# Optimization experiments

Measured on AMD Instinct MI355X. Metric: run time of the kernel, lower is better.

The kernel has to match this reference:

```python
import jax, jax.numpy as jnp
import numpy as np

EMBED_DIM = 1024
NUM_HEADS = 16
HEAD_DIM = EMBED_DIM // NUM_HEADS
SCALE = HEAD_DIM ** -0.5
B, S = 2, 2048


def setup_inputs() -> dict:
    key = jax.random.key(0)
    ks = jax.random.split(key, 11)
    lim = 1.0 / np.sqrt(EMBED_DIM)
    def lin(kw, kb):
        W = jax.random.uniform(kw, (EMBED_DIM, EMBED_DIM), jnp.float32, -lim, lim)
        b = jax.random.uniform(kb, (EMBED_DIM,), jnp.float32, -lim, lim)
        return W, b
    Wq, bq = lin(ks[0], ks[1])
    Wk, bk = lin(ks[2], ks[3])
    Wv, bv = lin(ks[4], ks[5])
    Wo, bo = lin(ks[6], ks[7])
    query = jax.random.normal(ks[8], (B, S, EMBED_DIM), jnp.float32)
    key_t = jax.random.normal(ks[9], (B, S, EMBED_DIM), jnp.float32)
    value = jax.random.normal(ks[10], (B, S, EMBED_DIM), jnp.float32)
    return {"query": query, "key": key_t, "value": value,
            "Wq": Wq, "bq": bq, "Wk": Wk, "bk": bk,
            "Wv": Wv, "bv": bv, "Wo": Wo, "bo": bo}


def reference(query, key, value, Wq, bq, Wk, bk, Wv, bv, Wo, bo):
    # 'flash' path with attn_mask=None == full softmax attention (chunking is
    # only an execution schedule; per-chunk softmax is over the full key axis).
    b, s, _ = query.shape
    def heads(x, W, bias):
        y = x @ W.T + bias                      # [b, s, E]
        return y.reshape(b, s, NUM_HEADS, HEAD_DIM).transpose(0, 2, 1, 3)  # [b, h, s, d]
    q = heads(query, Wq, bq)
    k = heads(key, Wk, bk)
    v = heads(value, Wv, bv)
    scores = jnp.einsum('bhqd,bhkd->bhqk', q, k) * SCALE
    attn = jax.nn.softmax(scores, axis=-1)
    out = jnp.einsum('bhqk,bhkd->bhqd', attn, v)
    out = out.transpose(0, 2, 1, 3).reshape(b, s, EMBED_DIM)
    return out @ Wo.T + bo
```

## Files before the change

kernel.cpp:

```cpp
#include <hip/hip_runtime.h>

typedef unsigned short u16;
typedef unsigned int u32;
typedef __attribute__((ext_vector_type(8))) __bf16 bf16x8;
typedef __attribute__((ext_vector_type(4))) float f32x4;
typedef __attribute__((ext_vector_type(4))) unsigned short u16x4;
typedef __attribute__((ext_vector_type(8))) unsigned short u16x8;
typedef __attribute__((ext_vector_type(2))) unsigned int u32x2;
typedef __attribute__((ext_vector_type(4))) unsigned int u32x4;

#define DEV static __device__ __forceinline__

DEV void async_copy16(const void* g, void* l) {
  __builtin_amdgcn_global_load_lds((const __attribute__((address_space(1))) void*)g,
                                   (__attribute__((address_space(3))) void*)l, 16, 0, 0);
}
DEV float b2f(u16 s) { union { unsigned u; float f; } v; v.u = ((unsigned)s) << 16; return v.f; }
DEV u16 f2b(float f) {
  union { float f; unsigned u; } v; v.f = f;
  unsigned r = v.u + 0x7FFFu + ((v.u >> 16) & 1u);
  return (u16)(r >> 16);
}
DEV u32 pack2bf(float a, float b) {
  u32 ua = __float_as_uint(a) + 0x8000u;
  u32 ub = __float_as_uint(b) + 0x8000u;
  return __builtin_amdgcn_perm(ub, ua, 0x07060302u);
}

#define MFMA(a, b, c) __builtin_amdgcn_mfma_f32_16x16x32_bf16((a), (b), (c), 0, 0, 0)

__global__ void detect_dtype(const unsigned* __restrict__ q, int* __restrict__ flag) {
  const int lane = threadIdx.x;
  const unsigned w = q[lane];
  const unsigned e = (w >> 7) & 0xFFu;
  const bool inr = (e >= 100u && e <= 132u);
  const unsigned long long m = __ballot(inr);
  if (lane == 0) flag[0] = (__popcll(m) >= 48) ? 1 : 0;
}

__global__ void convert_inputs(
    const void* s0, const void* s1, const void* s2,
    const void* s3, const void* s4, const void* s5, const void* s6,
    const void* s7, const void* s8, const void* s9, const void* s10,
    u16* __restrict__ d0, u16* __restrict__ d1, u16* __restrict__ d2,
    u16* __restrict__ d3, u16* __restrict__ d4, u16* __restrict__ d5, u16* __restrict__ d6,
    float* __restrict__ e7, float* __restrict__ e8, float* __restrict__ e9, float* __restrict__ e10,
    const int* __restrict__ flag)
{
  const int bi = blockIdx.y;
  const void* src = nullptr; u16* db = nullptr; float* df = nullptr; int n = 0;
  switch (bi) {
    case 0:  src = s0;  db = d0; n = 4194304; break;
    case 1:  src = s1;  db = d1; n = 4194304; break;
    case 2:  src = s2;  db = d2; n = 4194304; break;
    case 3:  src = s3;  db = d3; n = 1048576; break;
    case 4:  src = s4;  db = d4; n = 1048576; break;
    case 5:  src = s5;  db = d5; n = 1048576; break;
    case 6:  src = s6;  db = d6; n = 1048576; break;
    case 7:  src = s7;  df = e7; n = 1024; break;
    case 8:  src = s8;  df = e8; n = 1024; break;
    case 9:  src = s9;  df = e9; n = 1024; break;
    default: src = s10; df = e10; n = 1024; break;
  }
  const int isbf = flag[0];
  const int stride = gridDim.x * 256 * 8;
  for (int i = (blockIdx.x * 256 + threadIdx.x) * 8; i < n; i += stride) {
    if (db) {
      u16x8 v;
      if (isbf) {
        v = *(const u16x8*)((const u16*)src + i);
      } else {
        const float* sf = (const float*)src;
#pragma unroll
        for (int j = 0; j < 8; ++j) v[j] = f2b(sf[i + j]);
      }
      *(u16x8*)(db + i) = v;
    } else {
#pragma unroll
      for (int j = 0; j < 8; ++j) {
        float x = isbf ? b2f(((const u16*)src)[i + j]) : ((const float*)src)[i + j];
        df[i + j] = x;
      }
    }
  }
}

__global__ void gemm_qkv(const u16* __restrict__ X0, const u16* __restrict__ X1, const u16* __restrict__ X2,
                         const u16* __restrict__ W0, const u16* __restrict__ W1, const u16* __restrict__ W2,
                         const float* __restrict__ B0, const float* __restrict__ B1, const float* __restrict__ B2,
                         u16* __restrict__ Y0, u16* __restrict__ Y1, u16* __restrict__ Y2,
                         float* __restrict__ Yf, const int* __restrict__ flag, int mode0)
{
  __shared__ __align__(16) u16 smem[17408];

  const int z = blockIdx.z;
  const u16* X  = (z == 0) ? X0 : ((z == 1) ? X1 : X2);
  const u16* W  = (z == 0) ? W0 : ((z == 1) ? W1 : W2);
  const float* Bi = (z == 0) ? B0 : ((z == 1) ? B1 : B2);
  u16* Y        = (z == 0) ? Y0 : ((z == 1) ? Y1 : Y2);
  const int mode = mode0 ? mode0 : z;
  const int outbf = flag[0];

  const int t = threadIdx.x, wave = t >> 6, lane = t & 63;
  const int lane15 = lane & 15, quad = lane >> 4;

  const int L = blockIdx.y * 8 + blockIdx.x;
  const int wrk = (L & 7) * 32 + (L >> 3);
  const int m0 = (wrk >> 3) * 128, n0 = (wrk & 7) * 128;

  const u16* gA = X + (size_t)(m0 + wave * 16 + (lane >> 2)) * 1024 + (lane & 3) * 8;
  const u16* gB = W + (size_t)(n0 + wave * 16 + (lane >> 2)) * 1024 + (lane & 3) * 8;

  f32x4 acc[4][4];
#pragma unroll
  for (int i = 0; i < 4; ++i)
#pragma unroll
    for (int j = 0; j < 4; ++j) acc[i][j] = (f32x4){0.f, 0.f, 0.f, 0.f};

  const int wr = wave >> 1, wc = wave & 1;

  u16* lA0 = smem + wave * 512;
  u16* lB0 = smem + 4096 + wave * 512;
  u16* lA1 = smem + 8192 + wave * 512;
  u16* lB1 = smem + 12288 + wave * 512;

  auto stage = [&](u16* lA, u16* lB) {
    async_copy16(gA, lA);
    async_copy16(gA + 64 * 1024, lA + 64 * 32);
    async_copy16(gB, lB);
    async_copy16(gB + 64 * 1024, lB + 64 * 32);
    gA += 32; gB += 32;
  };
  auto compute = [&](const u16* As_, const u16* Bs_) {
    bf16x8 af[4], bfv[4];
#pragma unroll
    for (int mt = 0; mt < 4; ++mt)
      af[mt] = *(const bf16x8*)&As_[(wr * 64 + mt * 16 + lane15) * 32 + quad * 8];
#pragma unroll
    for (int nt = 0; nt < 4; ++nt)
      bfv[nt] = *(const bf16x8*)&Bs_[(wc * 64 + nt * 16 + lane15) * 32 + quad * 8];
    __builtin_amdgcn_s_setprio(1);
#pragma unroll
    for (int mt = 0; mt < 4; ++mt)
#pragma unroll
      for (int nt = 0; nt < 4; ++nt)
        acc[mt][nt] = MFMA(af[mt], bfv[nt], acc[mt][nt]);
    __builtin_amdgcn_s_setprio(0);
  };

  stage(lA0, lB0);
  __syncthreads();

  for (int k0 = 0; k0 < 1024; k0 += 64) {
    if (k0 + 32 < 1024) stage(lA1, lB1);
    compute(smem, smem + 4096);
    __syncthreads();
    if (k0 + 64 < 1024) stage(lA0, lB0);
    compute(smem + 8192, smem + 12288);
    __syncthreads();
  }

  const float qscale = 0.125f * 1.44269504088896340736f;

  if (mode == 2) {
    u16* T2 = smem;
#pragma unroll
    for (int mt = 0; mt < 4; ++mt) {
      const int sl_base = wr * 64 + mt * 16 + quad * 4;
#pragma unroll
      for (int nt = 0; nt < 4; ++nt) {
        const int nn = wc * 64 + nt * 16 + lane15;
        const float bias_v = Bi[n0 + nn];
#pragma unroll
        for (int r = 0; r < 4; ++r) {
          const int sl = sl_base + r;
          T2[nn * 136 + sl] = f2b(acc[mt][nt][r] + bias_v);
        }
      }
    }
    __syncthreads();
    const size_t grow0 = (size_t)(m0 >> 11) * 1024 + n0;
    const int col0 = m0 & 2047;
#pragma unroll
    for (int i = 0; i < 8; ++i) {
      const int id = i * 256 + t;
      const int row = id >> 4, ch = id & 15;
      *(u16x8*)&Y[(grow0 + row) * 2048 + col0 + ch * 8] = *(const u16x8*)&T2[row * 136 + ch * 8];
    }
    return;
  }

#pragma unroll
  for (int mt = 0; mt < 4; ++mt) {
    const int m_base = m0 + wr * 64 + mt * 16 + quad * 4;
#pragma unroll
    for (int nt = 0; nt < 4; ++nt) {
      const int n = n0 + wc * 64 + nt * 16 + lane15;
      const float bias_v = Bi[n];
#pragma unroll
      for (int r = 0; r < 4; ++r) {
        const int m = m_base + r;
        float v = acc[mt][nt][r] + bias_v;
        if (mode == 0) v *= qscale;
        if (mode == 3) {
          if (outbf) Y[(size_t)m * 1024 + n] = f2b(v);
          else       Yf[(size_t)m * 1024 + n] = v;
        } else {
          size_t addr = (((size_t)(m >> 11) * 16 + (n >> 6)) * 2048 + (size_t)(m & 2047)) * 64 + (n & 63);
          Y[addr] = f2b(v);
        }
      }
    }
  }
}

__global__ __launch_bounds__(256, 4) void flash_attn(const u16* __restrict__ Qs, const u16* __restrict__ Ks,
                                                     const u16* __restrict__ Vt, u16* __restrict__ AO)
{
  __shared__ __align__(16) u16 smem[16384];
  u16* Kt = smem;
  u16* Vs = smem + 8192;

  const int t = threadIdx.x, wave = t >> 6, lane = t & 63;
  const int lane15 = lane & 15, quad = lane >> 4;
  const int l7 = lane15 & 7;

  const int Lb = blockIdx.y * 16 + blockIdx.x;
  const int wrk = (Lb & 7) * 64 + (Lb >> 3);
  const int bh = wrk >> 4;
  const int q0 = (wrk & 15) * 128;

  const u16* Qb = Qs + ((size_t)bh * 2048 + q0) * 64;
  const u16* Kb = Ks + (size_t)bh * 2048 * 64;
  const u16* Vb = Vt + (size_t)bh * 64 * 2048;

  const int krow = lane >> 3;
  const int kchunk = (lane & 7) ^ (krow & 7);
  const int vrow = lane >> 4;
  const int vchunk = (lane & 15) ^ (((wave & 1) << 2) + vrow);

#pragma unroll
  for (int r = 0; r < 4; ++r)
    async_copy16(Qb + (size_t)(r * 32 + wave * 8 + krow) * 64 + kchunk * 8,
                 &Kt[(r * 32 + wave * 8) * 64]);
  __syncthreads();
  bf16x8 aq[2][2];
#pragma unroll
  for (int mt = 0; mt < 2; ++mt)
#pragma unroll
    for (int ks = 0; ks < 2; ++ks)
      aq[mt][ks] = *(const bf16x8*)&Kt[(wave * 32 + mt * 16 + lane15) * 64 + ((ks * 4 + quad) ^ l7) * 8];
  __syncthreads();

  f32x4 acc_o[2][4], acc_l[2];
#pragma unroll
  for (int mt = 0; mt < 2; ++mt) {
    acc_l[mt] = (f32x4){0.f, 0.f, 0.f, 0.f};
#pragma unroll
    for (int i = 0; i < 4; ++i) acc_o[mt][i] = (f32x4){0.f, 0.f, 0.f, 0.f};
  }

  u16x8 ou;
#pragma unroll
  for (int j = 0; j < 8; ++j) ou[j] = 0x3F80;
  const bf16x8 ones = __builtin_bit_cast(bf16x8, ou);

  for (int kt = 0; kt < 16; ++kt) {
#pragma unroll
    for (int r = 0; r < 4; ++r)
      async_copy16(Kb + (size_t)(kt * 128 + r * 32 + wave * 8 + krow) * 64 + kchunk * 8,
                   &Kt[(r * 32 + wave * 8) * 64]);
#pragma unroll
    for (int r = 0; r < 4; ++r)
      async_copy16(Vb + (size_t)(r * 16 + wave * 4 + vrow) * 2048 + kt * 128 + vchunk * 8,
                   &Vs[(r * 16 + wave * 4) * 128]);
    __syncthreads();

#pragma unroll
    for (int ks2 = 0; ks2 < 4; ++ks2) {
      bf16x8 bk[2][2];
#pragma unroll
      for (int no = 0; no < 2; ++no)
#pragma unroll
        for (int ks = 0; ks < 2; ++ks)
          bk[no][ks] = *(const bf16x8*)&Kt[((ks2 * 2 + no) * 16 + lane15) * 64 + ((ks * 4 + quad) ^ l7) * 8];
      f32x4 s2[2][2];
#pragma unroll
      for (int mt = 0; mt < 2; ++mt)
#pragma unroll
        for (int no = 0; no < 2; ++no) s2[mt][no] = (f32x4){0.f, 0.f, 0.f, 0.f};
      __builtin_amdgcn_s_setprio(1);
#pragma unroll
      for (int mt = 0; mt < 2; ++mt)
#pragma unroll
        for (int no = 0; no < 2; ++no)
#pragma unroll
          for (int ks = 0; ks < 2; ++ks)
            s2[mt][no] = MFMA(bk[no][ks], aq[mt][ks], s2[mt][no]);
      __builtin_amdgcn_s_setprio(0);

      bf16x8 pa[2];
#pragma unroll
      for (int mt = 0; mt < 2; ++mt) {
        float e0[4], e1[4];
#pragma unroll
        for (int rg = 0; rg < 4; ++rg) {
          e0[rg] = __builtin_amdgcn_exp2f(s2[mt][0][rg]);
          e1[rg] = __builtin_amdgcn_exp2f(s2[mt][1][rg]);
        }
        const u32 x0 = pack2bf(e0[0], e0[1]), x1 = pack2bf(e0[2], e0[3]);
        const u32 y0 = pack2bf(e1[0], e1[1]), y1 = pack2bf(e1[2], e1[3]);
        const u32x2 rA = __builtin_amdgcn_permlane32_swap(x0, y0, false, false);
        const u32x2 rB = __builtin_amdgcn_permlane32_swap(x1, y1, false, false);
        const u32x2 f0 = __builtin_amdgcn_permlane16_swap(rA[0], rA[1], false, false);
        const u32x2 f1 = __builtin_amdgcn_permlane16_swap(rB[0], rB[1], false, false);
        const u32x4 paw = (u32x4){f0[0], f1[0], f0[1], f1[1]};
        pa[mt] = __builtin_bit_cast(bf16x8, paw);
      }

      bf16x8 bv[4];
#pragma unroll
      for (int dt = 0; dt < 4; ++dt)
        bv[dt] = *(const bf16x8*)&Vs[(dt * 16 + lane15) * 128 + ((ks2 * 4 + quad) ^ l7) * 8];
      __builtin_amdgcn_s_setprio(1);
#pragma unroll
      for (int mt = 0; mt < 2; ++mt) {
#pragma unroll
        for (int dt = 0; dt < 4; ++dt)
          acc_o[mt][dt] = MFMA(pa[mt], bv[dt], acc_o[mt][dt]);
        acc_l[mt] = MFMA(pa[mt], ones, acc_l[mt]);
      }
      __builtin_amdgcn_s_setprio(0);
    }
    __syncthreads();
  }

  float rinv[2][4];
#pragma unroll
  for (int mt = 0; mt < 2; ++mt)
#pragma unroll
    for (int rg = 0; rg < 4; ++rg) rinv[mt][rg] = 1.0f / acc_l[mt][rg];

  u16* T = smem;
#pragma unroll
  for (int mt = 0; mt < 2; ++mt)
#pragma unroll
    for (int dt = 0; dt < 4; ++dt)
#pragma unroll
      for (int rg = 0; rg < 4; ++rg)
        T[(wave * 32 + mt * 16 + quad * 4 + rg) * 72 + dt * 16 + lane15] =
            f2b(acc_o[mt][dt][rg] * rinv[mt][rg]);
  __syncthreads();

  const int b = bh >> 4, h = bh & 15;
#pragma unroll
  for (int i = 0; i < 4; ++i) {
    const int id = i * 256 + t;
    const int row = id >> 3, ch = id & 7;
    *(u16x8*)&AO[((size_t)b * 2048 + q0 + row) * 1024 + h * 64 + ch * 8] =
        *(const u16x8*)&T[row * 72 + ch * 8];
  }
}

extern "C" void kernel_launch(void* const* d_in, const int* in_sizes, int n_in,
                              void* d_out, int out_size, void* d_ws, size_t ws_size,
                              hipStream_t stream)
{
  const void* query = d_in[0];
  const void* key_  = d_in[1];
  const void* value = d_in[2];
  const void* Wq = d_in[3]; const void* bq = d_in[4];
  const void* Wk = d_in[5]; const void* bk = d_in[6];
  const void* Wv = d_in[7]; const void* bv = d_in[8];
  const void* Wo = d_in[9]; const void* bo = d_in[10];

  u16* ws = (u16*)d_ws;
  u16* Qs  = ws;
  u16* Ks  = Qs + 4194304;
  u16* Vt  = Ks + 4194304;
  u16* AO  = Vt + 4194304;
  u16* Xq  = AO + 4194304;
  u16* Xk  = Xq + 4194304;
  u16* Xv  = Xk + 4194304;
  u16* Wqc = Xv + 4194304;
  u16* Wkc = Wqc + 1048576;
  u16* Wvc = Wkc + 1048576;
  u16* Woc = Wvc + 1048576;
  float* Bc = (float*)(Woc + 1048576);
  int* flag = (int*)(Bc + 4096);

  detect_dtype<<<1, 64, 0, stream>>>((const unsigned*)query, flag);
  convert_inputs<<<dim3(128, 11), 256, 0, stream>>>(
      query, key_, value, Wq, Wk, Wv, Wo, bq, bk, bv, bo,
      Xq, Xk, Xv, Wqc, Wkc, Wvc, Woc,
      Bc, Bc + 1024, Bc + 2048, Bc + 3072, flag);

  gemm_qkv<<<dim3(8, 32, 3), 256, 0, stream>>>(Xq, Xk, Xv, Wqc, Wkc, Wvc,
                                               Bc, Bc + 1024, Bc + 2048,
                                               Qs, Ks, Vt, nullptr, flag, 0);
  flash_attn<<<dim3(16, 32), 256, 0, stream>>>(Qs, Ks, Vt, AO);
  gemm_qkv<<<dim3(8, 32, 1), 256, 0, stream>>>(AO, AO, AO, Woc, Woc, Woc,
                                               Bc + 3072, Bc + 3072, Bc + 3072,
                                               (u16*)d_out, (u16*)d_out, (u16*)d_out,
                                               (float*)d_out, flag, 3);
}
```

Before: 221.8 us.

## Split attention key tiles across wave pairs with doubled query rows per wave

Each wave now owns 64 query rows (instead of 32) and half of each 128-key tile. A pair of waves shares the same query rows and their partial O and row sums are reduced through shared memory at the end. This halves the K/V fragment LDS reads per unit of MFMA work, raising reuse of the loaded K and V fragments. In exchange it needs roughly double the accumulator registers (launch bounds lowered to 2 blocks per CU) and adds an end-of-kernel reduction with extra barriers.

```diff
diff --git a/kernel.cpp b/kernel.cpp
--- a/kernel.cpp
+++ b/kernel.cpp
@@ -214,7 +214,7 @@
   }
 }
 
-__global__ __launch_bounds__(256, 4) void flash_attn(const u16* __restrict__ Qs, const u16* __restrict__ Ks,
+__global__ __launch_bounds__(256, 2) void flash_attn(const u16* __restrict__ Qs, const u16* __restrict__ Ks,
                                                      const u16* __restrict__ Vt, u16* __restrict__ AO)
 {
   __shared__ __align__(16) u16 smem[16384];
@@ -224,6 +224,8 @@
   const int t = threadIdx.x, wave = t >> 6, lane = t & 63;
   const int lane15 = lane & 15, quad = lane >> 4;
   const int l7 = lane15 & 7;
+  const int h = wave >> 1;
+  const int c = wave & 1;
 
   const int Lb = blockIdx.y * 16 + blockIdx.x;
   const int wrk = (Lb & 7) * 64 + (Lb >> 3);
@@ -244,17 +246,18 @@
     async_copy16(Qb + (size_t)(r * 32 + wave * 8 + krow) * 64 + kchunk * 8,
                  &Kt[(r * 32 + wave * 8) * 64]);
   __syncthreads();
-  bf16x8 aq[2][2];
-#pragma unroll
-  for (int mt = 0; mt < 2; ++mt)
+  bf16x8 aq[4][2];
+#pragma unroll
+  for (int mt = 0; mt < 4; ++mt)
 #pragma unroll
     for (int ks = 0; ks < 2; ++ks)
-      aq[mt][ks] = *(const bf16x8*)&Kt[(wave * 32 + mt * 16 + lane15) * 64 + ((ks * 4 + quad) ^ l7) * 8];
-  __syncthreads();
-
-  f32x4 acc_o[2][4], acc_l[2];
-#pragma unroll
-  for (int mt = 0; mt < 2; ++mt) {
+      aq[mt][ks] = *(const bf16x8*)&Kt[(h * 64 + mt * 16 + lane15) * 64 + ((ks * 4 + quad) ^ l7) * 8];
+  __syncthreads();
+
+  f32x4 acc_o[4][4];
+  f32x4 acc_l[4];
+#pragma unroll
+  for (int mt = 0; mt < 4; ++mt) {
     acc_l[mt] = (f32x4){0.f, 0.f, 0.f, 0.f};
 #pragma unroll
     for (int i = 0; i < 4; ++i) acc_o[mt][i] = (f32x4){0.f, 0.f, 0.f, 0.f};
@@ -277,36 +280,34 @@
     __syncthreads();
 
 #pragma unroll
-    for (int ks2 = 0; ks2 < 4; ++ks2) {
+    for (int g = 0; g < 2; ++g) {
+      const int ks2 = c * 2 + g;
       bf16x8 bk[2][2];
 #pragma unroll
       for (int no = 0; no < 2; ++no)
 #pragma unroll
         for (int ks = 0; ks < 2; ++ks)
-          bk[no][ks] = *(const bf16x8*)&Kt[((ks2 * 2 + no) * 16 + lane15) * 64 + ((ks * 4 + quad) ^ l7) * 8];
-      f32x4 s2[2][2];
-#pragma unroll
-      for (int mt = 0; mt < 2; ++mt)
-#pragma unroll
-        for (int no = 0; no < 2; ++no) s2[mt][no] = (f32x4){0.f, 0.f, 0.f, 0.f};
-      __builtin_amdgcn_s_setprio(1);
-#pragma unroll
-      for (int mt = 0; mt < 2; ++mt)
+          bk[no][ks] = *(const bf16x8*)&Kt[(c * 64 + g * 32 + no * 16 + lane15) * 64 + ((ks * 4 + quad) ^ l7) * 8];
+
+      bf16x8 pa[4];
+#pragma unroll
+      for (int mt = 0; mt < 4; ++mt) {
+        f32x4 s2[2];
+        s2[0] = (f32x4){0.f, 0.f, 0.f, 0.f};
+        s2[1] = (f32x4){0.f, 0.f, 0.f, 0.f};
+        __builtin_amdgcn_s_setprio(1);
 #pragma unroll
         for (int no = 0; no < 2; ++no)
 #pragma unroll
           for (int ks = 0; ks < 2; ++ks)
-            s2[mt][no] = MFMA(bk[no][ks], aq[mt][ks], s2[mt][no]);
-      __builtin_amdgcn_s_setprio(0);
-
-      bf16x8 pa[2];
-#pragma unroll
-      for (int mt = 0; mt < 2; ++mt) {
+            s2[no] = MFMA(bk[no][ks], aq[mt][ks], s2[no]);
+        __builtin_amdgcn_s_setprio(0);
+
         float e0[4], e1[4];
 #pragma unroll
         for (int rg = 0; rg < 4; ++rg) {
-          e0[rg] = __builtin_amdgcn_exp2f(s2[mt][0][rg]);
-          e1[rg] = __builtin_amdgcn_exp2f(s2[mt][1][rg]);
+          e0[rg] = __builtin_amdgcn_exp2f(s2[0][rg]);
+          e1[rg] = __builtin_amdgcn_exp2f(s2[1][rg]);
         }
         const u32 x0 = pack2bf(e0[0], e0[1]), x1 = pack2bf(e0[2], e0[3]);
         const u32 y0 = pack2bf(e1[0], e1[1]), y1 = pack2bf(e1[2], e1[3]);
@@ -324,7 +325,7 @@
         bv[dt] = *(const bf16x8*)&Vs[(dt * 16 + lane15) * 128 + ((ks2 * 4 + quad) ^ l7) * 8];
       __builtin_amdgcn_s_setprio(1);
 #pragma unroll
-      for (int mt = 0; mt < 2; ++mt) {
+      for (int mt = 0; mt < 4; ++mt) {
 #pragma unroll
         for (int dt = 0; dt < 4; ++dt)
           acc_o[mt][dt] = MFMA(pa[mt], bv[dt], acc_o[mt][dt]);
@@ -335,29 +336,65 @@
     __syncthreads();
   }
 
-  float rinv[2][4];
-#pragma unroll
-  for (int mt = 0; mt < 2; ++mt)
-#pragma unroll
-    for (int rg = 0; rg < 4; ++rg) rinv[mt][rg] = 1.0f / acc_l[mt][rg];
+  float* Of = (float*)smem;
+  if (c == 1) {
+#pragma unroll
+    for (int mt = 0; mt < 4; ++mt)
+#pragma unroll
+      for (int dt = 0; dt < 4; ++dt)
+#pragma unroll
+        for (int rg = 0; rg < 4; ++rg)
+          Of[h * 4096 + (mt * 16 + quad * 4 + rg) * 64 + dt * 16 + lane15] = acc_o[mt][dt][rg];
+  }
+  __syncthreads();
+  if (c == 0) {
+#pragma unroll
+    for (int mt = 0; mt < 4; ++mt)
+#pragma unroll
+      for (int dt = 0; dt < 4; ++dt)
+#pragma unroll
+        for (int rg = 0; rg < 4; ++rg)
+          acc_o[mt][dt][rg] += Of[h * 4096 + (mt * 16 + quad * 4 + rg) * 64 + dt * 16 + lane15];
+  }
+  __syncthreads();
+  float* Lf = (float*)smem;
+  if (c == 1 && lane15 == 0) {
+#pragma unroll
+    for (int mt = 0; mt < 4; ++mt)
+#pragma unroll
+      for (int rg = 0; rg < 4; ++rg)
+        Lf[h * 64 + mt * 16 + quad * 4 + rg] = acc_l[mt][rg];
+  }
+  __syncthreads();
+  float rinv[4][4];
+  if (c == 0) {
+#pragma unroll
+    for (int mt = 0; mt < 4; ++mt)
+#pragma unroll
+      for (int rg = 0; rg < 4; ++rg)
+        rinv[mt][rg] = 1.0f / (acc_l[mt][rg] + Lf[h * 64 + mt * 16 + quad * 4 + rg]);
+  }
+  __syncthreads();
 
   u16* T = smem;
-#pragma unroll
-  for (int mt = 0; mt < 2; ++mt)
-#pragma unroll
-    for (int dt = 0; dt < 4; ++dt)
-#pragma unroll
-      for (int rg = 0; rg < 4; ++rg)
-        T[(wave * 32 + mt * 16 + quad * 4 + rg) * 72 + dt * 16 + lane15] =
-            f2b(acc_o[mt][dt][rg] * rinv[mt][rg]);
-  __syncthreads();
-
-  const int b = bh >> 4, h = bh & 15;
+  if (c == 0) {
+#pragma unroll
+    for (int mt = 0; mt < 4; ++mt)
+#pragma unroll
+      for (int dt = 0; dt < 4; ++dt)
+#pragma unroll
+        for (int rg = 0; rg < 4; ++rg)
+          T[(h * 64 + mt * 16 + quad * 4 + rg) * 72 + dt * 16 + lane15] =
+              f2b(acc_o[mt][dt][rg] * rinv[mt][rg]);
+  }
+  __syncthreads();
+
+  const int b = bh >> 4, hh = bh & 15;
 #pragma unroll
   for (int i = 0; i < 4; ++i) {
     const int id = i * 256 + t;
     const int row = id >> 3, ch = id & 7;
-    *(u16x8*)&AO[((size_t)b * 2048 + q0 + row) * 1024 + h * 64 + ch * 8] =
+    *(u16x8*)&AO[((size_t)b * 2048 + q0 + row) * 1024 + hh * 64 + ch * 8] =
         *(const u16x8*)&T[row * 72 + ch * 8];
   }
 }
```

New measurement: 219.8 us. About the same (-0.9%).
